# Optimization experiments

Measured on AMD Instinct MI355X. Metric: run time of the kernel, lower is better.

Reference implementation:

```python
import jax, jax.numpy as jnp
import numpy as np

B, S, D = 4, 2048, 1024
H, DK, DV = 16, 64, 64
NEG = -1e10


def setup_inputs() -> dict:
    key = jax.random.key(0)
    ks = jax.random.split(key, 7)
    queries = jax.random.normal(ks[0], (B, S, D), dtype=jnp.float32)
    keys = jax.random.normal(ks[1], (B, S, D), dtype=jnp.float32)
    values = jax.random.normal(ks[2], (B, S, D), dtype=jnp.float32)
    mask = jnp.ones((B, S, S), dtype=jnp.int32)
    # per-head Linear weights, torch layout [out, in]; stacked over heads
    Wq = jax.random.normal(ks[3], (H, DK, D), dtype=jnp.float32) / np.sqrt(D)
    Wk = jax.random.normal(ks[4], (H, DK, D), dtype=jnp.float32) / np.sqrt(D)
    Wv = jax.random.normal(ks[5], (H, DV, D), dtype=jnp.float32) / np.sqrt(D)
    Wo = jax.random.normal(ks[6], (D, H * DV), dtype=jnp.float32) / np.sqrt(H * DV)
    return {"queries": queries, "keys": keys, "values": values, "mask": mask,
            "Wq": Wq, "Wk": Wk, "Wv": Wv, "Wo": Wo}


def reference(queries, keys, values, mask, Wq, Wk, Wv, Wo):
    # per-head projections, vectorized over heads: y = x @ W_h^T
    q = jnp.einsum('bsd,hkd->bhsk', queries, Wq)   # [B,H,S,DK]
    k = jnp.einsum('btd,hkd->bhtk', keys, Wk)      # [B,H,S,DK]
    v = jnp.einsum('btd,hvd->bhtv', values, Wv)    # [B,H,S,DV]
    scores = jnp.einsum('bhsk,bhtk->bhst', q, k) / jnp.sqrt(jnp.asarray(DK, q.dtype))
    scores = jnp.where(mask[:, None, :, :] == 0, jnp.asarray(NEG, q.dtype), scores)
    attn = jax.nn.softmax(scores, axis=-1)
    out = jnp.einsum('bhst,bhtv->bhsv', attn, v)   # [B,H,S,DV]
    # torch.cat over heads on last dim == head-major concat per position
    out = out.transpose(0, 2, 1, 3).reshape(B, S, H * DV)
    return out @ Wo.T
```

## Files before the change

kernel.cpp:

```cpp
#include <hip/hip_runtime.h>
#include <stdint.h>

typedef __attribute__((ext_vector_type(4))) float f32x4;
typedef __attribute__((ext_vector_type(8))) __bf16 bf16x8;
typedef __attribute__((ext_vector_type(4))) __bf16 bf16x4;
typedef __attribute__((ext_vector_type(4))) short s16x4;
typedef __attribute__((ext_vector_type(2))) uint32_t u32x2;

#define MFMA16(a, b, c) __builtin_amdgcn_mfma_f32_16x16x32_bf16(a, b, c, 0, 0, 0)
#define MFMA16K16(a, b, c) __builtin_amdgcn_mfma_f32_16x16x16bf16_1k(a, b, c, 0, 0, 0)

#define B_ 4
#define S_ 2048
#define D_ 1024
#define H_ 16
#define NEG_ -1e10f

__device__ __forceinline__ void glds16(const void* gsrc, void* ldst) {
  __builtin_amdgcn_global_load_lds(
      (__attribute__((address_space(1))) void*)(gsrc),
      (__attribute__((address_space(3))) void*)(ldst),
      16, 0, 0);
}

__device__ __forceinline__ uint32_t pack_bf16(float a, float b) {
  uint32_t ua = (uint32_t)__builtin_bit_cast(unsigned short, (__bf16)a);
  uint32_t ub = (uint32_t)__builtin_bit_cast(unsigned short, (__bf16)b);
  return ua | (ub << 16);
}

__global__ __launch_bounds__(256) void cvt3(const float* __restrict__ a, const float* __restrict__ b,
                                            const float* __restrict__ c, __bf16* __restrict__ oa,
                                            __bf16* __restrict__ ob, __bf16* __restrict__ oc) {
  const float* in; __bf16* out;
  if (blockIdx.z == 0) { in = a; out = oa; }
  else if (blockIdx.z == 1) { in = b; out = ob; }
  else { in = c; out = oc; }
  int i = (blockIdx.x * 256 + threadIdx.x) * 4;
  float4 v = *(const float4*)(in + i);
  bf16x4 o;
  o.x = (__bf16)v.x; o.y = (__bf16)v.y; o.z = (__bf16)v.z; o.w = (__bf16)v.w;
  *(bf16x4*)(out + i) = o;
}

__global__ __launch_bounds__(256) void cvt4(const float* __restrict__ a, const float* __restrict__ b,
                                            const float* __restrict__ c, const float* __restrict__ d,
                                            __bf16* __restrict__ oa, __bf16* __restrict__ ob,
                                            __bf16* __restrict__ oc, __bf16* __restrict__ od) {
  const float* in; __bf16* out;
  if (blockIdx.z == 0) { in = a; out = oa; }
  else if (blockIdx.z == 1) { in = b; out = ob; }
  else if (blockIdx.z == 2) { in = c; out = oc; }
  else { in = d; out = od; }
  int i = (blockIdx.x * 256 + threadIdx.x) * 4;
  float4 v = *(const float4*)(in + i);
  bf16x4 o;
  o.x = (__bf16)v.x; o.y = (__bf16)v.y; o.z = (__bf16)v.z; o.w = (__bf16)v.w;
  *(bf16x4*)(out + i) = o;
}

__global__ __launch_bounds__(256) void mask_pack(const int* __restrict__ mask,
                                                 uint32_t* __restrict__ bits,
                                                 int* __restrict__ flags) {
  int tt = blockIdx.x, st = blockIdx.y, b = blockIdx.z;
  int tid = threadIdx.x, w = tid >> 6, lane = tid & 63;
  __shared__ int andred;
  if (tid == 0) andred = 1;
  __syncthreads();
  unsigned long long all1 = ~0ull;
  for (int rr = 0; rr < 32; rr++) {
    int srow = st * 128 + w * 32 + rr;
    #pragma unroll
    for (int half = 0; half < 2; half++) {
      int c = tt * 128 + half * 64 + lane;
      int m = mask[((size_t)b * S_ + srow) * S_ + c];
      unsigned long long bal = __ballot(m != 0);
      all1 &= bal;
      if (lane == 0) {
        uint32_t* dst = &bits[((size_t)b * S_ + srow) * 64 + tt * 4 + half * 2];
        dst[0] = (uint32_t)bal;
        dst[1] = (uint32_t)(bal >> 32);
      }
    }
  }
  if (all1 != ~0ull) atomicAnd(&andred, 0);
  __syncthreads();
  if (tid == 0) flags[(b * 16 + st) * 16 + tt] = andred;
}

template <int MODE>
__global__ __launch_bounds__(256, 2) void gemm_bt(
    const __bf16* __restrict__ A0, const __bf16* __restrict__ A1, const __bf16* __restrict__ A2,
    const __bf16* __restrict__ W0, const __bf16* __restrict__ W1, const __bf16* __restrict__ W2,
    void* O0, void* O1, void* O2) {
  const int K = 1024;
  const __bf16* PA; const __bf16* PB; void* O;
  int pa_t, pb_t;
  if (MODE == 0) {
    if (blockIdx.z == 0)      { PA = W0; PB = A0; O = O0; pa_t = blockIdx.x; pb_t = blockIdx.y; }
    else if (blockIdx.z == 1) { PA = W1; PB = A1; O = O1; pa_t = blockIdx.x; pb_t = blockIdx.y; }
    else                      { PA = A2; PB = W2; O = O2; pa_t = blockIdx.y; pb_t = blockIdx.x; }
  } else { PA = A0; PB = W0; O = O0; pa_t = blockIdx.y; pb_t = blockIdx.x; }

  __shared__ __align__(16) __bf16 As[128 * 64];
  __shared__ __align__(16) __bf16 Bs[128 * 64];
  int tid = threadIdx.x, lane = tid & 63, w = tid >> 6;
  int wm = w >> 1, wn = w & 1;
  int g = lane >> 4, l15 = lane & 15;
  f32x4 acc[4][4] = {};
  const __bf16* Ablk = PA + (size_t)(pa_t * 128) * K;
  const __bf16* Bblk = PB + (size_t)(pb_t * 128) * K;

  for (int kt = 0; kt < K; kt += 64) {
    __syncthreads();
    #pragma unroll
    for (int r = 0; r < 4; r++) {
      int C = r * 256 + tid;
      int row = C >> 3, c = C & 7;
      int c0 = c ^ (row & 7);
      glds16(Ablk + (size_t)row * K + kt + c0 * 8, (char*)As + C * 16);
      glds16(Bblk + (size_t)row * K + kt + c0 * 8, (char*)Bs + C * 16);
    }
    __syncthreads();
    #pragma unroll
    for (int kkq = 0; kkq < 2; kkq++) {
      bf16x8 af[4], bfr[4];
      #pragma unroll
      for (int i = 0; i < 4; i++) {
        int row = wm * 64 + i * 16 + l15;
        int ch = (kkq * 4 + g) ^ (row & 7);
        af[i] = *(const bf16x8*)((const char*)As + row * 128 + ch * 16);
      }
      #pragma unroll
      for (int j = 0; j < 4; j++) {
        int row = wn * 64 + j * 16 + l15;
        int ch = (kkq * 4 + g) ^ (row & 7);
        bfr[j] = *(const bf16x8*)((const char*)Bs + row * 128 + ch * 16);
      }
      #pragma unroll
      for (int i = 0; i < 4; i++)
        #pragma unroll
        for (int j = 0; j < 4; j++)
          acc[i][j] = MFMA16(af[i], bfr[j], acc[i][j]);
    }
  }

  if (MODE == 1) {
    #pragma unroll
    for (int i = 0; i < 4; i++)
      #pragma unroll
      for (int j = 0; j < 4; j++)
        #pragma unroll
        for (int r = 0; r < 4; r++) {
          int m = pa_t * 128 + wm * 64 + i * 16 + g * 4 + r;
          int n = pb_t * 128 + wn * 64 + j * 16 + l15;
          ((float*)O)[(size_t)m * 1024 + n] = acc[i][j][r];
        }
  } else if (blockIdx.z == 2) {
    #pragma unroll
    for (int i = 0; i < 4; i++)
      #pragma unroll
      for (int j = 0; j < 4; j++) {
        int s0 = pa_t * 128 + wm * 64 + i * 16 + g * 4;
        int dvg = pb_t * 128 + wn * 64 + j * 16 + l15;
        int b = s0 >> 11, s = s0 & 2047;
        int h = dvg >> 6, dv = dvg & 63;
        bf16x4 o;
        #pragma unroll
        for (int r = 0; r < 4; r++) o[r] = (__bf16)acc[i][j][r];
        *(bf16x4*)((__bf16*)O + (((size_t)b * 16 + h) * 64 + dv) * 2048 + s) = o;
      }
  } else {
    float scale = (blockIdx.z == 0) ? 0.125f : 1.0f;
    #pragma unroll
    for (int i = 0; i < 4; i++)
      #pragma unroll
      for (int j = 0; j < 4; j++) {
        int dkg = pa_t * 128 + wm * 64 + i * 16 + g * 4;
        int sg = pb_t * 128 + wn * 64 + j * 16 + l15;
        int h = dkg >> 6, dk = dkg & 63;
        int b = sg >> 11, s = sg & 2047;
        bf16x4 o;
        #pragma unroll
        for (int r = 0; r < 4; r++) o[r] = (__bf16)(acc[i][j][r] * scale);
        *(bf16x4*)((__bf16*)O + (((size_t)b * 16 + h) * 2048 + s) * 64 + dk) = o;
      }
  }
}

__global__ __launch_bounds__(256, 3) void attn(
    const __bf16* __restrict__ qp, const __bf16* __restrict__ kp,
    const __bf16* __restrict__ vt_, __bf16* __restrict__ aout,
    const uint32_t* __restrict__ bits, const int* __restrict__ flags) {
  int qt = blockIdx.x, bh = blockIdx.y, b = bh >> 4, h = bh & 15;
  int tid = threadIdx.x, lane = tid & 63, w = tid >> 6;
  int g = lane >> 4, l15 = lane & 15;

  __shared__ __align__(16) char smem[32768];
  char* Klds = smem;
  char* Vlds = smem + 16384;

  const __bf16* Qg = qp + ((size_t)bh * S_ + qt * 128) * 64;
  const __bf16* Kg = kp + (size_t)bh * S_ * 64;
  const __bf16* Vg = vt_ + (size_t)bh * 64 * S_;

  #pragma unroll
  for (int r = 0; r < 4; r++) {
    int C = r * 256 + tid;
    int row = C >> 3, c = C & 7, c0 = c ^ (row & 7);
    glds16(Qg + row * 64 + c0 * 8, Klds + C * 16);
  }
  __syncthreads();
  bf16x8 qf[2][2];
  #pragma unroll
  for (int i = 0; i < 2; i++)
    #pragma unroll
    for (int kkq = 0; kkq < 2; kkq++) {
      int row = w * 32 + i * 16 + l15;
      int ch = (kkq * 4 + g) ^ (row & 7);
      qf[i][kkq] = *(const bf16x8*)(Klds + row * 128 + ch * 16);
    }
  __syncthreads();

  f32x4 oacc[4][2] = {};
  float mst[2] = {-INFINITY, -INFINITY}, lst[2] = {0.f, 0.f};

  for (int kt = 0; kt < 16; kt++) {
    const __bf16* Ks = Kg + (size_t)kt * 128 * 64;
    #pragma unroll
    for (int r = 0; r < 4; r++) {
      int C = r * 256 + tid;
      int row = C >> 3, c = C & 7, c0 = c ^ (row & 7);
      glds16(Ks + row * 64 + c0 * 8, Klds + C * 16);
    }
    #pragma unroll
    for (int r = 0; r < 4; r++) {
      int C = r * 256 + tid;
      int row = C >> 4, c = C & 15;
      int c0 = (c & 8) | ((c & 7) ^ (row & 7));
      glds16(Vg + (size_t)row * S_ + kt * 128 + c0 * 8, Vlds + C * 16);
    }
    __syncthreads();

    int flag = flags[(b * 16 + qt) * 16 + kt];

    #pragma unroll
    for (int hh = 0; hh < 2; hh++) {
      f32x4 sacc[2][4] = {};
      #pragma unroll
      for (int jt = 0; jt < 4; jt++) {
        int row = (hh * 4 + jt) * 16 + l15;
        bf16x8 kf0 = *(const bf16x8*)(Klds + row * 128 + (g ^ (row & 7)) * 16);
        bf16x8 kf1 = *(const bf16x8*)(Klds + row * 128 + ((4 + g) ^ (row & 7)) * 16);
        sacc[0][jt] = MFMA16(kf0, qf[0][0], sacc[0][jt]);
        sacc[0][jt] = MFMA16(kf1, qf[0][1], sacc[0][jt]);
        sacc[1][jt] = MFMA16(kf0, qf[1][0], sacc[1][jt]);
        sacc[1][jt] = MFMA16(kf1, qf[1][1], sacc[1][jt]);
      }

      if (!flag) {
        #pragma unroll
        for (int i = 0; i < 2; i++) {
          int srow = qt * 128 + w * 32 + i * 16 + l15;
          const uint32_t* bw = &bits[((size_t)b * S_ + srow) * 64 + kt * 4 + hh * 2];
          uint32_t m0 = bw[0], m1 = bw[1];
          #pragma unroll
          for (int jt = 0; jt < 4; jt++) {
            uint32_t mw = (jt & 2) ? m1 : m0;
            #pragma unroll
            for (int r = 0; r < 4; r++) {
              int bitpos = (jt & 1) * 16 + g * 4 + r;
              if (!((mw >> bitpos) & 1)) sacc[i][jt][r] = NEG_;
            }
          }
        }
      }

      s16x4 pf[2][4];
      float alpha[2];
      #pragma unroll
      for (int i = 0; i < 2; i++) {
        float mx = -INFINITY;
        #pragma unroll
        for (int jt = 0; jt < 4; jt++)
          #pragma unroll
          for (int r = 0; r < 4; r++) mx = fmaxf(mx, sacc[i][jt][r]);
        mx = fmaxf(mx, __shfl_xor(mx, 16));
        mx = fmaxf(mx, __shfl_xor(mx, 32));
        float mnew = fmaxf(mst[i], mx);
        alpha[i] = __expf(mst[i] - mnew);
        mst[i] = mnew;
        float sum = 0.f;
        #pragma unroll
        for (int jt = 0; jt < 4; jt++) {
          float p0 = __expf(sacc[i][jt][0] - mnew);
          float p1 = __expf(sacc[i][jt][1] - mnew);
          float p2 = __expf(sacc[i][jt][2] - mnew);
          float p3 = __expf(sacc[i][jt][3] - mnew);
          sum += (p0 + p1) + (p2 + p3);
          u32x2 t;
          t.x = pack_bf16(p0, p1);
          t.y = pack_bf16(p2, p3);
          pf[i][jt] = __builtin_bit_cast(s16x4, t);
        }
        sum += __shfl_xor(sum, 16);
        sum += __shfl_xor(sum, 32);
        lst[i] = lst[i] * alpha[i] + sum;
      }
      #pragma unroll
      for (int vt = 0; vt < 4; vt++)
        #pragma unroll
        for (int i = 0; i < 2; i++)
          #pragma unroll
          for (int r = 0; r < 4; r++) oacc[vt][i][r] *= alpha[i];

      #pragma unroll
      for (int jt = 0; jt < 4; jt++) {
        int ch = (hh * 4 + jt) * 2 + (g >> 1);
        #pragma unroll
        for (int vt = 0; vt < 4; vt++) {
          int row = vt * 16 + l15;
          int chs = (ch & 8) | ((ch & 7) ^ (row & 7));
          s16x4 vv = *(const s16x4*)(Vlds + row * 256 + chs * 16 + (g & 1) * 8);
          oacc[vt][0] = MFMA16K16(vv, pf[0][jt], oacc[vt][0]);
          oacc[vt][1] = MFMA16K16(vv, pf[1][jt], oacc[vt][1]);
        }
      }
    }
    __syncthreads();
  }

  #pragma unroll
  for (int i = 0; i < 2; i++) {
    float inv = 1.0f / lst[i];
    int srow = qt * 128 + w * 32 + i * 16 + l15;
    #pragma unroll
    for (int vt = 0; vt < 4; vt++) {
      bf16x4 o;
      #pragma unroll
      for (int r = 0; r < 4; r++) o[r] = (__bf16)(oacc[vt][i][r] * inv);
      *(bf16x4*)(aout + ((size_t)b * S_ + srow) * 1024 + h * 64 + vt * 16 + g * 4) = o;
    }
  }
}

extern "C" void kernel_launch(void* const* d_in, const int* in_sizes, int n_in,
                              void* d_out, int out_size, void* d_ws, size_t ws_size,
                              hipStream_t stream) {
  const float* queries = (const float*)d_in[0];
  const float* keys    = (const float*)d_in[1];
  const float* values  = (const float*)d_in[2];
  const int*   mask    = (const int*)d_in[3];
  const float* Wq      = (const float*)d_in[4];
  const float* Wk      = (const float*)d_in[5];
  const float* Wv      = (const float*)d_in[6];
  const float* Wo      = (const float*)d_in[7];

  char* ws = (char*)d_ws;
  __bf16* Xq  = (__bf16*)(ws + 0);
  __bf16* Xk  = (__bf16*)(ws + 16777216);
  __bf16* Xv  = (__bf16*)(ws + 33554432);
  __bf16* Wqb = (__bf16*)(ws + 50331648);
  __bf16* Wkb = (__bf16*)(ws + 52428800);
  __bf16* Wvb = (__bf16*)(ws + 54525952);
  __bf16* Wob = (__bf16*)(ws + 56623104);
  __bf16* qp  = (__bf16*)(ws + 58720256);
  __bf16* kp  = (__bf16*)(ws + 75497472);
  __bf16* vT  = (__bf16*)(ws + 92274688);
  uint32_t* bits = (uint32_t*)(ws + 109051904);
  int* flags     = (int*)(ws + 111149056);
  __bf16* aout = Xq;

  cvt3<<<dim3(8192, 1, 3), 256, 0, stream>>>(queries, keys, values, Xq, Xk, Xv);
  cvt4<<<dim3(1024, 1, 4), 256, 0, stream>>>(Wq, Wk, Wv, Wo, Wqb, Wkb, Wvb, Wob);

  mask_pack<<<dim3(16, 16, 4), 256, 0, stream>>>(mask, bits, flags);

  gemm_bt<0><<<dim3(8, 64, 3), 256, 0, stream>>>(Xq, Xk, Xv, Wqb, Wkb, Wvb,
                                                 (void*)qp, (void*)kp, (void*)vT);

  attn<<<dim3(16, 64), 256, 0, stream>>>(qp, kp, vT, aout, bits, flags);

  gemm_bt<1><<<dim3(8, 64, 1), 256, 0, stream>>>(aout, nullptr, nullptr, Wob, nullptr, nullptr,
                                                 (void*)d_out, nullptr, nullptr);
}
```

Before: 438.0 us.

## Fuse prep kernels, use exp2 softmax, widen attention tile, vectorize output stores

Merges the three conversion and mask-packing launches into one prep kernel to cut launch overhead. Folds log2(e) into the Q scale so softmax can use the hardware exp2, and processes all 128 keys of a tile in one online-softmax step, so each tile does one max/rescale instead of two. Swaps the operand roles in the final projection GEMM so each lane stores a contiguous f32x4 instead of scattered scalars. The wider score tile raises register pressure in the attention kernel.

```diff
diff --git a/kernel.cpp b/kernel.cpp
--- a/kernel.cpp
+++ b/kernel.cpp
@@ -15,6 +15,9 @@
 #define D_ 1024
 #define H_ 16
 #define NEG_ -1e10f
+#define QSCALE 0.180336880f
+
+__device__ __forceinline__ float ex2(float x) { return __builtin_amdgcn_exp2f(x); }
 
 __device__ __forceinline__ void glds16(const void* gsrc, void* ldst) {
   __builtin_amdgcn_global_load_lds(
@@ -29,63 +32,61 @@
   return ua | (ub << 16);
 }
 
-__global__ __launch_bounds__(256) void cvt3(const float* __restrict__ a, const float* __restrict__ b,
-                                            const float* __restrict__ c, __bf16* __restrict__ oa,
-                                            __bf16* __restrict__ ob, __bf16* __restrict__ oc) {
-  const float* in; __bf16* out;
-  if (blockIdx.z == 0) { in = a; out = oa; }
-  else if (blockIdx.z == 1) { in = b; out = ob; }
-  else { in = c; out = oc; }
-  int i = (blockIdx.x * 256 + threadIdx.x) * 4;
-  float4 v = *(const float4*)(in + i);
-  bf16x4 o;
-  o.x = (__bf16)v.x; o.y = (__bf16)v.y; o.z = (__bf16)v.z; o.w = (__bf16)v.w;
-  *(bf16x4*)(out + i) = o;
-}
-
-__global__ __launch_bounds__(256) void cvt4(const float* __restrict__ a, const float* __restrict__ b,
-                                            const float* __restrict__ c, const float* __restrict__ d,
-                                            __bf16* __restrict__ oa, __bf16* __restrict__ ob,
-                                            __bf16* __restrict__ oc, __bf16* __restrict__ od) {
-  const float* in; __bf16* out;
-  if (blockIdx.z == 0) { in = a; out = oa; }
-  else if (blockIdx.z == 1) { in = b; out = ob; }
-  else if (blockIdx.z == 2) { in = c; out = oc; }
-  else { in = d; out = od; }
-  int i = (blockIdx.x * 256 + threadIdx.x) * 4;
-  float4 v = *(const float4*)(in + i);
-  bf16x4 o;
-  o.x = (__bf16)v.x; o.y = (__bf16)v.y; o.z = (__bf16)v.z; o.w = (__bf16)v.w;
-  *(bf16x4*)(out + i) = o;
-}
-
-__global__ __launch_bounds__(256) void mask_pack(const int* __restrict__ mask,
-                                                 uint32_t* __restrict__ bits,
-                                                 int* __restrict__ flags) {
-  int tt = blockIdx.x, st = blockIdx.y, b = blockIdx.z;
-  int tid = threadIdx.x, w = tid >> 6, lane = tid & 63;
+__global__ __launch_bounds__(256) void prep(
+    const float* __restrict__ xq, const float* __restrict__ xk, const float* __restrict__ xv,
+    const float* __restrict__ wq, const float* __restrict__ wk, const float* __restrict__ wv,
+    const float* __restrict__ wo,
+    __bf16* __restrict__ oxq, __bf16* __restrict__ oxk, __bf16* __restrict__ oxv,
+    __bf16* __restrict__ owq, __bf16* __restrict__ owk, __bf16* __restrict__ owv,
+    __bf16* __restrict__ owo,
+    const int* __restrict__ mask, uint32_t* __restrict__ bits, int* __restrict__ flags) {
+  int bid = blockIdx.x, tid = threadIdx.x;
   __shared__ int andred;
-  if (tid == 0) andred = 1;
-  __syncthreads();
-  unsigned long long all1 = ~0ull;
-  for (int rr = 0; rr < 32; rr++) {
-    int srow = st * 128 + w * 32 + rr;
-    #pragma unroll
-    for (int half = 0; half < 2; half++) {
-      int c = tt * 128 + half * 64 + lane;
-      int m = mask[((size_t)b * S_ + srow) * S_ + c];
-      unsigned long long bal = __ballot(m != 0);
-      all1 &= bal;
-      if (lane == 0) {
-        uint32_t* dst = &bits[((size_t)b * S_ + srow) * 64 + tt * 4 + half * 2];
-        dst[0] = (uint32_t)bal;
-        dst[1] = (uint32_t)(bal >> 32);
-      }
-    }
-  }
-  if (all1 != ~0ull) atomicAnd(&andred, 0);
-  __syncthreads();
-  if (tid == 0) flags[(b * 16 + st) * 16 + tt] = andred;
+  if (bid < 24576) {
+    int z = bid >> 13, xb = bid & 8191;
+    const float* in = (z == 0) ? xq : (z == 1) ? xk : xv;
+    __bf16* out = (z == 0) ? oxq : (z == 1) ? oxk : oxv;
+    int i = (xb * 256 + tid) * 4;
+    float4 v = *(const float4*)(in + i);
+    bf16x4 o;
+    o.x = (__bf16)v.x; o.y = (__bf16)v.y; o.z = (__bf16)v.z; o.w = (__bf16)v.w;
+    *(bf16x4*)(out + i) = o;
+  } else if (bid < 28672) {
+    int m = bid - 24576;
+    int z = m >> 10, wb = m & 1023;
+    const float* in = (z == 0) ? wq : (z == 1) ? wk : (z == 2) ? wv : wo;
+    __bf16* out = (z == 0) ? owq : (z == 1) ? owk : (z == 2) ? owv : owo;
+    int i = (wb * 256 + tid) * 4;
+    float4 v = *(const float4*)(in + i);
+    bf16x4 o;
+    o.x = (__bf16)v.x; o.y = (__bf16)v.y; o.z = (__bf16)v.z; o.w = (__bf16)v.w;
+    *(bf16x4*)(out + i) = o;
+  } else {
+    int m = bid - 28672;
+    int tt = m & 15, st = (m >> 4) & 15, b = m >> 8;
+    int w = tid >> 6, lane = tid & 63;
+    if (tid == 0) andred = 1;
+    __syncthreads();
+    unsigned long long all1 = ~0ull;
+    for (int rr = 0; rr < 32; rr++) {
+      int srow = st * 128 + w * 32 + rr;
+      #pragma unroll
+      for (int half = 0; half < 2; half++) {
+        int c = tt * 128 + half * 64 + lane;
+        int mm = mask[((size_t)b * S_ + srow) * S_ + c];
+        unsigned long long bal = __ballot(mm != 0);
+        all1 &= bal;
+        if (lane == 0) {
+          uint32_t* dst = &bits[((size_t)b * S_ + srow) * 64 + tt * 4 + half * 2];
+          dst[0] = (uint32_t)bal;
+          dst[1] = (uint32_t)(bal >> 32);
+        }
+      }
+    }
+    if (all1 != ~0ull) atomicAnd(&andred, 0);
+    __syncthreads();
+    if (tid == 0) flags[(b * 16 + st) * 16 + tt] = andred;
+  }
 }
 
 template <int MODE>
@@ -100,7 +101,7 @@
     if (blockIdx.z == 0)      { PA = W0; PB = A0; O = O0; pa_t = blockIdx.x; pb_t = blockIdx.y; }
     else if (blockIdx.z == 1) { PA = W1; PB = A1; O = O1; pa_t = blockIdx.x; pb_t = blockIdx.y; }
     else                      { PA = A2; PB = W2; O = O2; pa_t = blockIdx.y; pb_t = blockIdx.x; }
-  } else { PA = A0; PB = W0; O = O0; pa_t = blockIdx.y; pb_t = blockIdx.x; }
+  } else { PA = W0; PB = A0; O = O0; pa_t = blockIdx.x; pb_t = blockIdx.y; }
 
   __shared__ __align__(16) __bf16 As[128 * 64];
   __shared__ __align__(16) __bf16 Bs[128 * 64];
@@ -149,13 +150,11 @@
     #pragma unroll
     for (int i = 0; i < 4; i++)
       #pragma unroll
-      for (int j = 0; j < 4; j++)
-        #pragma unroll
-        for (int r = 0; r < 4; r++) {
-          int m = pa_t * 128 + wm * 64 + i * 16 + g * 4 + r;
-          int n = pb_t * 128 + wn * 64 + j * 16 + l15;
-          ((float*)O)[(size_t)m * 1024 + n] = acc[i][j][r];
-        }
+      for (int j = 0; j < 4; j++) {
+        int n0 = pa_t * 128 + wm * 64 + i * 16 + g * 4;
+        int m = pb_t * 128 + wn * 64 + j * 16 + l15;
+        *(f32x4*)((float*)O + (size_t)m * 1024 + n0) = acc[i][j];
+      }
   } else if (blockIdx.z == 2) {
     #pragma unroll
     for (int i = 0; i < 4; i++)
@@ -171,7 +170,7 @@
         *(bf16x4*)((__bf16*)O + (((size_t)b * 16 + h) * 64 + dv) * 2048 + s) = o;
       }
   } else {
-    float scale = (blockIdx.z == 0) ? 0.125f : 1.0f;
+    float scale = (blockIdx.z == 0) ? QSCALE : 1.0f;
     #pragma unroll
     for (int i = 0; i < 4; i++)
       #pragma unroll
@@ -242,90 +241,86 @@
     }
     __syncthreads();
 
-    int flag = flags[(b * 16 + qt) * 16 + kt];
-
-    #pragma unroll
-    for (int hh = 0; hh < 2; hh++) {
-      f32x4 sacc[2][4] = {};
-      #pragma unroll
-      for (int jt = 0; jt < 4; jt++) {
-        int row = (hh * 4 + jt) * 16 + l15;
-        bf16x8 kf0 = *(const bf16x8*)(Klds + row * 128 + (g ^ (row & 7)) * 16);
-        bf16x8 kf1 = *(const bf16x8*)(Klds + row * 128 + ((4 + g) ^ (row & 7)) * 16);
-        sacc[0][jt] = MFMA16(kf0, qf[0][0], sacc[0][jt]);
-        sacc[0][jt] = MFMA16(kf1, qf[0][1], sacc[0][jt]);
-        sacc[1][jt] = MFMA16(kf0, qf[1][0], sacc[1][jt]);
-        sacc[1][jt] = MFMA16(kf1, qf[1][1], sacc[1][jt]);
-      }
-
-      if (!flag) {
-        #pragma unroll
-        for (int i = 0; i < 2; i++) {
-          int srow = qt * 128 + w * 32 + i * 16 + l15;
-          const uint32_t* bw = &bits[((size_t)b * S_ + srow) * 64 + kt * 4 + hh * 2];
-          uint32_t m0 = bw[0], m1 = bw[1];
+    f32x4 sacc[2][8] = {};
+    #pragma unroll
+    for (int jt = 0; jt < 8; jt++) {
+      int row = jt * 16 + l15;
+      bf16x8 kf0 = *(const bf16x8*)(Klds + row * 128 + (g ^ (row & 7)) * 16);
+      bf16x8 kf1 = *(const bf16x8*)(Klds + row * 128 + ((4 + g) ^ (row & 7)) * 16);
+      sacc[0][jt] = MFMA16(kf0, qf[0][0], sacc[0][jt]);
+      sacc[0][jt] = MFMA16(kf1, qf[0][1], sacc[0][jt]);
+      sacc[1][jt] = MFMA16(kf0, qf[1][0], sacc[1][jt]);
+      sacc[1][jt] = MFMA16(kf1, qf[1][1], sacc[1][jt]);
+    }
+
+    if (!flags[(b * 16 + qt) * 16 + kt]) {
+      #pragma unroll
+      for (int i = 0; i < 2; i++) {
+        int srow = qt * 128 + w * 32 + i * 16 + l15;
+        const uint32_t* bw = &bits[((size_t)b * S_ + srow) * 64 + kt * 4];
+        uint32_t mw[4] = {bw[0], bw[1], bw[2], bw[3]};
+        #pragma unroll
+        for (int jt = 0; jt < 8; jt++)
           #pragma unroll
-          for (int jt = 0; jt < 4; jt++) {
-            uint32_t mw = (jt & 2) ? m1 : m0;
-            #pragma unroll
-            for (int r = 0; r < 4; r++) {
-              int bitpos = (jt & 1) * 16 + g * 4 + r;
-              if (!((mw >> bitpos) & 1)) sacc[i][jt][r] = NEG_;
-            }
+          for (int r = 0; r < 4; r++) {
+            int bitpos = (jt & 1) * 16 + g * 4 + r;
+            if (!((mw[jt >> 1] >> bitpos) & 1)) sacc[i][jt][r] = NEG_;
           }
-        }
-      }
-
-      s16x4 pf[2][4];
-      float alpha[2];
+      }
+    }
+
+    float alpha[2];
+    #pragma unroll
+    for (int i = 0; i < 2; i++) {
+      float mx = -INFINITY;
+      #pragma unroll
+      for (int jt = 0; jt < 8; jt++)
+        #pragma unroll
+        for (int r = 0; r < 4; r++) mx = fmaxf(mx, sacc[i][jt][r]);
+      mx = fmaxf(mx, __shfl_xor(mx, 16));
+      mx = fmaxf(mx, __shfl_xor(mx, 32));
+      float mnew = fmaxf(mst[i], mx);
+      alpha[i] = ex2(mst[i] - mnew);
+      mst[i] = mnew;
+    }
+    #pragma unroll
+    for (int vt = 0; vt < 4; vt++)
+      #pragma unroll
+      for (int i = 0; i < 2; i++)
+        #pragma unroll
+        for (int r = 0; r < 4; r++) oacc[vt][i][r] *= alpha[i];
+
+    float sum[2] = {0.f, 0.f};
+    #pragma unroll
+    for (int jt = 0; jt < 8; jt++) {
+      s16x4 pf[2];
       #pragma unroll
       for (int i = 0; i < 2; i++) {
-        float mx = -INFINITY;
-        #pragma unroll
-        for (int jt = 0; jt < 4; jt++)
-          #pragma unroll
-          for (int r = 0; r < 4; r++) mx = fmaxf(mx, sacc[i][jt][r]);
-        mx = fmaxf(mx, __shfl_xor(mx, 16));
-        mx = fmaxf(mx, __shfl_xor(mx, 32));
-        float mnew = fmaxf(mst[i], mx);
-        alpha[i] = __expf(mst[i] - mnew);
-        mst[i] = mnew;
-        float sum = 0.f;
-        #pragma unroll
-        for (int jt = 0; jt < 4; jt++) {
-          float p0 = __expf(sacc[i][jt][0] - mnew);
-          float p1 = __expf(sacc[i][jt][1] - mnew);
-          float p2 = __expf(sacc[i][jt][2] - mnew);
-          float p3 = __expf(sacc[i][jt][3] - mnew);
-          sum += (p0 + p1) + (p2 + p3);
-          u32x2 t;
-          t.x = pack_bf16(p0, p1);
-          t.y = pack_bf16(p2, p3);
-          pf[i][jt] = __builtin_bit_cast(s16x4, t);
-        }
-        sum += __shfl_xor(sum, 16);
-        sum += __shfl_xor(sum, 32);
-        lst[i] = lst[i] * alpha[i] + sum;
-      }
-      #pragma unroll
-      for (int vt = 0; vt < 4; vt++)
-        #pragma unroll
-        for (int i = 0; i < 2; i++)
-          #pragma unroll
-          for (int r = 0; r < 4; r++) oacc[vt][i][r] *= alpha[i];
-
-      #pragma unroll
-      for (int jt = 0; jt < 4; jt++) {
-        int ch = (hh * 4 + jt) * 2 + (g >> 1);
-        #pragma unroll
-        for (int vt = 0; vt < 4; vt++) {
-          int row = vt * 16 + l15;
-          int chs = (ch & 8) | ((ch & 7) ^ (row & 7));
-          s16x4 vv = *(const s16x4*)(Vlds + row * 256 + chs * 16 + (g & 1) * 8);
-          oacc[vt][0] = MFMA16K16(vv, pf[0][jt], oacc[vt][0]);
-          oacc[vt][1] = MFMA16K16(vv, pf[1][jt], oacc[vt][1]);
-        }
-      }
+        float p0 = ex2(sacc[i][jt][0] - mst[i]);
+        float p1 = ex2(sacc[i][jt][1] - mst[i]);
+        float p2 = ex2(sacc[i][jt][2] - mst[i]);
+        float p3 = ex2(sacc[i][jt][3] - mst[i]);
+        sum[i] += (p0 + p1) + (p2 + p3);
+        u32x2 t;
+        t.x = pack_bf16(p0, p1);
+        t.y = pack_bf16(p2, p3);
+        pf[i] = __builtin_bit_cast(s16x4, t);
+      }
+      int ch = jt * 2 + (g >> 1);
+      #pragma unroll
+      for (int vt = 0; vt < 4; vt++) {
+        int row = vt * 16 + l15;
+        int chs = (ch & 8) | ((ch & 7) ^ (row & 7));
+        s16x4 vv = *(const s16x4*)(Vlds + row * 256 + chs * 16 + (g & 1) * 8);
+        oacc[vt][0] = MFMA16K16(vv, pf[0], oacc[vt][0]);
+        oacc[vt][1] = MFMA16K16(vv, pf[1], oacc[vt][1]);
+      }
+    }
+    #pragma unroll
+    for (int i = 0; i < 2; i++) {
+      sum[i] += __shfl_xor(sum[i], 16);
+      sum[i] += __shfl_xor(sum[i], 32);
+      lst[i] = lst[i] * alpha[i] + sum[i];
     }
     __syncthreads();
   }
@@ -371,10 +366,9 @@
   int* flags     = (int*)(ws + 111149056);
   __bf16* aout = Xq;
 
-  cvt3<<<dim3(8192, 1, 3), 256, 0, stream>>>(queries, keys, values, Xq, Xk, Xv);
-  cvt4<<<dim3(1024, 1, 4), 256, 0, stream>>>(Wq, Wk, Wv, Wo, Wqb, Wkb, Wvb, Wob);
-
-  mask_pack<<<dim3(16, 16, 4), 256, 0, stream>>>(mask, bits, flags);
+  prep<<<29696, 256, 0, stream>>>(queries, keys, values, Wq, Wk, Wv, Wo,
+                                  Xq, Xk, Xv, Wqb, Wkb, Wvb, Wob,
+                                  mask, bits, flags);
 
   gemm_bt<0><<<dim3(8, 64, 3), 256, 0, stream>>>(Xq, Xk, Xv, Wqb, Wkb, Wvb,
                                                  (void*)qp, (void*)kp, (void*)vT);
```

Result: slower. 569.4 us (+30.0%).
